# Kernel optimization log

Hardware: AMD Instinct MI355X
Metric: run time of the kernel (lower is better)

## Reference

```python
import jax, jax.numpy as jnp
import numpy as np

EPS = 1e-5
MODES = 64
KERNEL = 25
PRED = 336
N_ENC = 2

def rmsnorm(x, w):
    return x * jax.lax.rsqrt(jnp.mean(jnp.square(x), axis=-1, keepdims=True) + EPS) * w

def ffn(x, w1, b1, w2, b2):
    return jax.nn.gelu(x @ w1 + b1, approximate=False) @ w2 + b2

def series_decomp(x):
    # moving average with zero padding (Conv1d, kernel=KERNEL, weight=1/KERNEL)
    pad = (KERNEL - 1) // 2
    xp = jnp.pad(x, ((0, 0), (pad, pad), (0, 0)))
    cs = jnp.cumsum(xp, axis=1)
    cs = jnp.concatenate([jnp.zeros_like(cs[:, :1]), cs], axis=1)
    t = (cs[:, KERNEL:, :] - cs[:, :-KERNEL, :]) / KERNEL  # [B,T,C]
    return x - t, t

def fourier_block(x, w, nw):
    # x: [B,T,C]; w: [MODES,C,2] learned complex weights; nw: [C] rms scale
    B, T, C = x.shape
    Xf = jnp.fft.rfft(x, axis=1)                      # [B,F,C] complex64
    mag = jnp.sum(Xf[:, 1:].real**2 + Xf[:, 1:].imag**2, axis=-1)  # [B,F-1]
    K = min(MODES, Xf.shape[1] - 1)
    _, idx = jax.lax.top_k(mag, K)
    idx = idx + 1                                      # skip DC, [B,K]
    Xsel = jnp.take_along_axis(Xf, idx[:, :, None], axis=1)  # [B,K,C]
    Wc = w[:K, :, 0] + 1j * w[:K, :, 1]               # [K,C]
    Ysel = Xsel * Wc[None]                             # [B,K,C]
    Yf = jnp.zeros_like(Xf).at[jnp.arange(B)[:, None], idx].set(Ysel)
    y = jnp.fft.irfft(Yf, n=T, axis=1)                 # [B,T,C]
    return rmsnorm(y, nw)

def setup_inputs() -> dict:
    key = jax.random.key(0)
    ks = iter(jax.random.split(key, 64))
    B, L, Cin, Cout, D, FF = 32, 1024, 8, 8, 512, 2048
    r = lambda *s: jax.random.normal(next(ks), s, dtype=jnp.float32) * 0.02
    z = lambda *s: jnp.zeros(s, dtype=jnp.float32)
    o = lambda *s: jnp.ones(s, dtype=jnp.float32)
    return {
        'x': jax.random.normal(next(ks), (B, L, Cin), dtype=jnp.float32),
        'enc_in_w': r(Cin, D), 'enc_in_b': z(D),
        'dec_in_w': r(Cin, D), 'dec_in_b': z(D),
        'enc_freq_w': r(N_ENC, MODES, D, 2), 'enc_freq_nw': o(N_ENC, D),
        'enc_n1': o(N_ENC, D), 'enc_n2': o(N_ENC, D),
        'enc_w1': r(N_ENC, D, FF), 'enc_b1': z(N_ENC, FF),
        'enc_w2': r(N_ENC, FF, D), 'enc_b2': z(N_ENC, D),
        'dec_freq_w': r(MODES, D, 2), 'dec_freq_nw': o(D),
        'dec_n1': o(D), 'dec_n2': o(D), 'dec_nx': o(D),
        'dec_cross_w': r(D, D), 'dec_cross_b': z(D),
        'dec_w1': r(D, FF), 'dec_b1': z(FF),
        'dec_w2': r(FF, D), 'dec_b2': z(D),
        'seas_w': r(D, Cout), 'seas_b': z(Cout),
        'tr_w1': r(D, FF), 'tr_b1': z(FF),
        'tr_w2': r(FF, Cout), 'tr_b2': z(Cout),
        'mix_w': r(Cout, Cout), 'mix_b': z(Cout),
        'qpos': jax.random.normal(next(ks), (1, PRED, D), dtype=jnp.float32) * 0.02,
    }

def reference(x, enc_in_w, enc_in_b, dec_in_w, dec_in_b,
              enc_freq_w, enc_freq_nw, enc_n1, enc_n2, enc_w1, enc_b1, enc_w2, enc_b2,
              dec_freq_w, dec_freq_nw, dec_n1, dec_n2, dec_nx, dec_cross_w, dec_cross_b,
              dec_w1, dec_b1, dec_w2, dec_b2, seas_w, seas_b,
              tr_w1, tr_b1, tr_w2, tr_b2, mix_w, mix_b, qpos):
    s, t = series_decomp(x)
    sez = s @ enc_in_w + enc_in_b                      # [B,L,D]
    for i in range(N_ENC):
        sez = sez + fourier_block(rmsnorm(sez, enc_n1[i]), enc_freq_w[i], enc_freq_nw[i])
        sez = sez + ffn(rmsnorm(sez, enc_n2[i]), enc_w1[i], enc_b1[i], enc_w2[i], enc_b2[i])
    memory = sez
    tgt = qpos + sez[:, -1:, :]                        # [B,PRED,D]
    # decoder layer
    m = jnp.mean(memory, axis=1, keepdims=True)        # [B,1,D]
    m = rmsnorm(m, dec_nx) @ dec_cross_w + dec_cross_b
    y = fourier_block(rmsnorm(tgt, dec_n1), dec_freq_w, dec_freq_nw)
    xd = tgt + y * jax.nn.sigmoid(m)
    xd = xd + ffn(rmsnorm(xd, dec_n2), dec_w1, dec_b1, dec_w2, dec_b2)
    sez_out = xd @ seas_w + seas_b                     # [B,PRED,Cout]
    tr = t @ dec_in_w + dec_in_b
    tr_out = ffn(tr[:, -1:, :], tr_w1, tr_b1, tr_w2, tr_b2)  # [B,1,Cout], broadcasts
    out = sez_out + tr_out
    return out @ mix_w + mix_b
```

## Files before the change

### kernel.cpp

```cpp
#include <hip/hip_runtime.h>
#include <hip/hip_fp16.h>
#include <math.h>

#define B_    32
#define L_    1024
#define D_    512
#define FF_   2048
#define PRED_ 336
#define ME_   (B_*L_)
#define MD_   (B_*PRED_)
#define EPS_  1e-5f

typedef _Float16 f16;
typedef _Float16 f16x8 __attribute__((ext_vector_type(8)));
typedef float    f32x4 __attribute__((ext_vector_type(4)));

__device__ __forceinline__ float wred64(float v) {
#pragma unroll
  for (int o = 32; o > 0; o >>= 1) v += __shfl_xor(v, o, 64);
  return v;
}
__device__ __forceinline__ double dwred64(double v) {
#pragma unroll
  for (int o = 32; o > 0; o >>= 1) v += __shfl_xor(v, o, 64);
  return v;
}
__device__ __forceinline__ float gelu_f(float x) {
  return 0.5f * x * (1.0f + erff(x * 0.7071067811865476f));
}
__device__ __forceinline__ void gl2lds16(const void* g, void* l) {
  __builtin_amdgcn_global_load_lds((const __attribute__((address_space(1))) void*)g,
                                   (__attribute__((address_space(3))) void*)l, 16, 0, 0);
}

__global__ void k_transpose_cast(const float* __restrict__ in, f16* __restrict__ out, int R, int C) {
  __shared__ float t[32][33];
  int c0 = blockIdx.x * 32, r0 = blockIdx.y * 32;
  int tx = threadIdx.x, ty = threadIdx.y;
#pragma unroll
  for (int j = ty; j < 32; j += 8) t[j][tx] = in[(size_t)(r0 + j) * C + c0 + tx];
  __syncthreads();
#pragma unroll
  for (int j = ty; j < 32; j += 8) out[(size_t)(c0 + j) * R + r0 + tx] = (f16)t[tx][j];
}

__global__ __launch_bounds__(256) void k_decomp_proj(const float* __restrict__ x,
    const float* __restrict__ w, const float* __restrict__ bias, float* __restrict__ sez) {
  int b = blockIdx.x, t0 = blockIdx.y * 128, tid = threadIdx.x;
  __shared__ float xs[152][8];
  __shared__ float st[128][8];
  __shared__ float wsm[8 * 512];
  __shared__ float bs[512];
  for (int i = tid; i < 152 * 8; i += 256) {
    int tt = i >> 3, c = i & 7; int tg = t0 - 12 + tt;
    xs[tt][c] = (tg >= 0 && tg < 1024) ? x[((size_t)b * 1024 + tg) * 8 + c] : 0.0f;
  }
  for (int i = tid; i < 4096; i += 256) wsm[i] = w[i];
  for (int i = tid; i < 512; i += 256) bs[i] = bias[i];
  __syncthreads();
  for (int i = tid; i < 1024; i += 256) {
    int t = i >> 3, c = i & 7;
    float s = 0.f;
#pragma unroll
    for (int j = 0; j < 25; ++j) s += xs[t + j][c];
    st[t][c] = xs[t + 12][c] - s / 25.0f;
  }
  __syncthreads();
#pragma unroll
  for (int g = 0; g < 2; ++g) {
    int d = tid + g * 256;
    float wb[8];
#pragma unroll
    for (int c = 0; c < 8; ++c) wb[c] = wsm[c * 512 + d];
    float bb = bs[d];
    for (int t = 0; t < 128; ++t) {
      float o = bb;
#pragma unroll
      for (int c = 0; c < 8; ++c) o += st[t][c] * wb[c];
      sez[((size_t)b * 1024 + t0 + t) * 512 + d] = o;
    }
  }
}

__global__ __launch_bounds__(512) void k_trend_trin(const float* __restrict__ x, const float* __restrict__ w,
    const float* __restrict__ bias, float* __restrict__ trin) {
  int b = blockIdx.x, tid = threadIdx.x;
  __shared__ float tl[8];
  if (tid < 8) {
    float s = 0.f;
    for (int j = 1011; j <= 1023; ++j) s += x[((size_t)b * 1024 + j) * 8 + tid];
    tl[tid] = s / 25.0f;
  }
  __syncthreads();
  float acc = bias[tid];
#pragma unroll
  for (int c = 0; c < 8; ++c) acc += tl[c] * w[c * 512 + tid];
  trin[b * 512 + tid] = acc;
}

__global__ __launch_bounds__(256) void k_rinv(const float* __restrict__ xin, float* __restrict__ rinv) {
  int row = blockIdx.x * 4 + (threadIdx.x >> 6), lane = threadIdx.x & 63;
  const float4* p = (const float4*)(xin + (size_t)row * 512);
  float4 a = p[lane * 2], b = p[lane * 2 + 1];
  float ss = a.x*a.x + a.y*a.y + a.z*a.z + a.w*a.w + b.x*b.x + b.y*b.y + b.z*b.z + b.w*b.w;
  ss = wred64(ss);
  if (lane == 0) rinv[row] = rsqrtf(ss * (1.0f / 512.0f) + EPS_);
}

__global__ __launch_bounds__(256) void k_rms_f16(const float* __restrict__ xin, const float* __restrict__ w,
    f16* __restrict__ out) {
  int row = blockIdx.x * 4 + (threadIdx.x >> 6), lane = threadIdx.x & 63;
  const float4* p = (const float4*)(xin + (size_t)row * 512);
  float4 a = p[lane * 2], b = p[lane * 2 + 1];
  float ss = a.x*a.x + a.y*a.y + a.z*a.z + a.w*a.w + b.x*b.x + b.y*b.y + b.z*b.z + b.w*b.w;
  ss = wred64(ss);
  float ri = rsqrtf(ss * (1.0f / 512.0f) + EPS_);
  const float4* wp = (const float4*)w;
  float4 wa = wp[lane * 2], wb = wp[lane * 2 + 1];
  float va[8] = {a.x, a.y, a.z, a.w, b.x, b.y, b.z, b.w};
  float wv[8] = {wa.x, wa.y, wa.z, wa.w, wb.x, wb.y, wb.z, wb.w};
  f16x8 o;
#pragma unroll
  for (int j = 0; j < 8; ++j) o[j] = (f16)((va[j] * ri) * wv[j]);
  *(f16x8*)(out + (size_t)row * 512 + lane * 8) = o;
}

#define IDX_(i) ((i) + ((i) >> 4))
__global__ __launch_bounds__(256) void k_fft_enc(const float* __restrict__ sez, const float* __restrict__ rinv,
    const float* __restrict__ n1, float* __restrict__ Xf) {
  int b = blockIdx.x, c0 = blockIdx.y * 4, tid = threadIdx.x;
  __shared__ double Zr[2][1088], Zi[2][1088];
  __shared__ double TWr[256], TWi[256];
  if (tid < 256) {
    double a = -6.283185307179586232 * (double)tid / 1024.0;
    TWr[tid] = cos(a); TWi[tid] = sin(a);
  }
  for (int i = tid; i < 4096; i += 256) {
    int t = i >> 2, cl = i & 3;
    float xv = (sez[((size_t)b * 1024 + t) * 512 + c0 + cl] * rinv[b * 1024 + t]) * n1[c0 + cl];
    int u = t, rt = 0;
#pragma unroll
    for (int d = 0; d < 5; ++d) { rt = (rt << 2) | (u & 3); u >>= 2; }
    if (cl & 1) Zi[cl >> 1][IDX_(rt)] = (double)xv; else Zr[cl >> 1][IDX_(rt)] = (double)xv;
  }
  __syncthreads();
#pragma unroll
  for (int s = 0; s < 5; ++s) {
    const int lh = 2 * s, h = 1 << lh;
#pragma unroll
    for (int qi = 0; qi < 2; ++qi) {
      int q = tid + qi * 256;
      int p = q >> 8, qq = q & 255;
      int j = qq & (h - 1), g = qq >> lh;
      int p0 = (g << (lh + 2)) + j;
      int i0 = IDX_(p0), i1 = IDX_(p0 + h), i2 = IDX_(p0 + 2 * h), i3 = IDX_(p0 + 3 * h);
      int tw = j << (8 - lh);
      double w1r = TWr[tw], w1i = TWi[tw];
      double w2r = w1r * w1r - w1i * w1i, w2i = 2.0 * w1r * w1i;
      double w3r = w2r * w1r - w2i * w1i, w3i = w2r * w1i + w2i * w1r;
      double Ar = Zr[p][i0], Ai = Zi[p][i0];
      double br = Zr[p][i1], bi = Zi[p][i1];
      double cr = Zr[p][i2], ci = Zi[p][i2];
      double dr = Zr[p][i3], di = Zi[p][i3];
      double Br = br * w1r - bi * w1i, Bi = br * w1i + bi * w1r;
      double Cr = cr * w2r - ci * w2i, Ci = cr * w2i + ci * w2r;
      double Dr = dr * w3r - di * w3i, Di = dr * w3i + di * w3r;
      double T0r = Ar + Cr, T0i = Ai + Ci;
      double T1r = Ar - Cr, T1i = Ai - Ci;
      double T2r = Br + Dr, T2i = Bi + Di;
      double T3r = Bi - Di, T3i = Dr - Br;
      Zr[p][i0] = T0r + T2r; Zi[p][i0] = T0i + T2i;
      Zr[p][i1] = T1r + T3r; Zi[p][i1] = T1i + T3i;
      Zr[p][i2] = T0r - T2r; Zi[p][i2] = T0i - T2i;
      Zr[p][i3] = T1r - T3r; Zi[p][i3] = T1i - T3i;
    }
    __syncthreads();
  }
  for (int i = tid; i < 513 * 2; i += 256) {
    int f = i >> 1, p = i & 1;
    int mf = (1024 - f) & 1023;
    double Ar = Zr[p][IDX_(f)], Ai = Zi[p][IDX_(f)], Br = Zr[p][IDX_(mf)], Bi = Zi[p][IDX_(mf)];
    float4 o;
    o.x = (float)(0.5 * (Ar + Br)); o.y = (float)(0.5 * (Ai - Bi));
    o.z = (float)(0.5 * (Ai + Bi)); o.w = (float)(0.5 * (Br - Ar));
    *(float4*)&Xf[(((size_t)b * 513 + f) * 512 + c0 + 2 * p) * 2] = o;
  }
}

__global__ __launch_bounds__(256) void k_mag(const float* __restrict__ Xf, double* __restrict__ mag, int F) {
  int b = blockIdx.x, f = blockIdx.y + 1, tid = threadIdx.x;
  const float2* row = (const float2*)(Xf + ((size_t)b * F + f) * 512 * 2);
  double s = 0;
  for (int c = tid; c < 512; c += 256) { float2 v = row[c]; s += (double)v.x * v.x + (double)v.y * v.y; }
  s = dwred64(s);
  __shared__ double ps[4];
  if ((tid & 63) == 0) ps[tid >> 6] = s;
  __syncthreads();
  if (tid == 0) mag[b * 513 + f] = ps[0] + ps[1] + ps[2] + ps[3];
}

__global__ __launch_bounds__(256) void k_topk(const double* __restrict__ mag, int* __restrict__ idx, int F) {
  int b = blockIdx.x, tid = threadIdx.x;
  __shared__ double v[528];
  __shared__ double rv[256];
  __shared__ int ri[256];
  for (int s = tid; s < 528; s += 256) v[s] = (s >= 1 && s < F) ? mag[b * 513 + s] : -1e300;
  __syncthreads();
  for (int r = 0; r < 64; ++r) {
    double bv = -1e300; int bi = 0;
    for (int s = tid; s < 528; s += 256) { double xv = v[s]; if (xv > bv) { bv = xv; bi = s; } }
    rv[tid] = bv; ri[tid] = bi;
    __syncthreads();
    for (int st = 128; st > 0; st >>= 1) {
      if (tid < st) {
        double o = rv[tid + st]; int oi = ri[tid + st];
        if (o > rv[tid] || (o == rv[tid] && oi < ri[tid])) { rv[tid] = o; ri[tid] = oi; }
      }
      __syncthreads();
    }
    if (tid == 0) { idx[b * 64 + r] = ri[0]; v[ri[0]] = -1e300; }
    __syncthreads();
  }
}

__global__ __launch_bounds__(512) void k_gather(const float* __restrict__ Xf, const int* __restrict__ idx,
    const float* __restrict__ fw, float* __restrict__ Ysel, int F, int T) {
  int b = blockIdx.x, k = blockIdx.y, c = threadIdx.x;
  int f = idx[b * 64 + k];
  float sc = (2 * f == T) ? (1.0f / (float)T) : (2.0f / (float)T);
  float2 xv = *(const float2*)&Xf[(((size_t)b * F + f) * 512 + c) * 2];
  float wr = fw[(k * 512 + c) * 2], wi = fw[(k * 512 + c) * 2 + 1];
  float yr = (xv.x * wr - xv.y * wi) * sc;
  float yi = (xv.x * wi + xv.y * wr) * sc;
  *(float2*)&Ysel[((size_t)(b * 64 + k) * 512 + c) * 2] = make_float2(yr, yi);
}

template <int T>
__global__ __launch_bounds__(256) void k_irfft(const float* __restrict__ Ysel, const int* __restrict__ idx,
    const float* __restrict__ nw, const float* __restrict__ sig,
    float* __restrict__ dst, int mode) {
  int b = blockIdx.x, t0 = blockIdx.y * 16, tid = threadIdx.x;
  int cq = tid & 127;
  int tg = tid >> 7;
  __shared__ float tcT[16][68], tsT[16][68];
  __shared__ int sidx[64];
  __shared__ float red[4][8];
  __shared__ float rfac[16];
  if (tid < 64) sidx[tid] = idx[b * 64 + tid];
  __syncthreads();
  for (int i = tid; i < 1024; i += 256) {
    int k = i >> 4, tt = i & 15;
    int m = (sidx[k] * (t0 + tt)) % T;
    float ang = (float)m * (float)(6.283185307179586232 / (double)T);
    tcT[tt][k] = cosf(ang);
    tsT[tt][k] = sinf(ang);
  }
  __syncthreads();
  float acc[8][4];
#pragma unroll
  for (int q = 0; q < 8; ++q)
#pragma unroll
    for (int j = 0; j < 4; ++j) acc[q][j] = 0.f;
  const float4* ys = (const float4*)Ysel + (size_t)b * 64 * 256 + 2 * cq;
  for (int k4 = 0; k4 < 64; k4 += 4) {
    float4 ya[4], yb[4];
#pragma unroll
    for (int kk = 0; kk < 4; ++kk) {
      ya[kk] = ys[(size_t)(k4 + kk) * 256];
      yb[kk] = ys[(size_t)(k4 + kk) * 256 + 1];
    }
#pragma unroll
    for (int q = 0; q < 8; ++q) {
      int tt = tg * 8 + q;
      float4 c4 = *(const float4*)&tcT[tt][k4];
      float4 s4 = *(const float4*)&tsT[tt][k4];
      acc[q][0] += ya[0].x * c4.x - ya[0].y * s4.x;
      acc[q][1] += ya[0].z * c4.x - ya[0].w * s4.x;
      acc[q][2] += yb[0].x * c4.x - yb[0].y * s4.x;
      acc[q][3] += yb[0].z * c4.x - yb[0].w * s4.x;
      acc[q][0] += ya[1].x * c4.y - ya[1].y * s4.y;
      acc[q][1] += ya[1].z * c4.y - ya[1].w * s4.y;
      acc[q][2] += yb[1].x * c4.y - yb[1].y * s4.y;
      acc[q][3] += yb[1].z * c4.y - yb[1].w * s4.y;
      acc[q][0] += ya[2].x * c4.z - ya[2].y * s4.z;
      acc[q][1] += ya[2].z * c4.z - ya[2].w * s4.z;
      acc[q][2] += yb[2].x * c4.z - yb[2].y * s4.z;
      acc[q][3] += yb[2].z * c4.z - yb[2].w * s4.z;
      acc[q][0] += ya[3].x * c4.w - ya[3].y * s4.w;
      acc[q][1] += ya[3].z * c4.w - ya[3].w * s4.w;
      acc[q][2] += yb[3].x * c4.w - yb[3].y * s4.w;
      acc[q][3] += yb[3].z * c4.w - yb[3].w * s4.w;
    }
  }
  int lane = tid & 63, wv = tid >> 6;
#pragma unroll
  for (int q = 0; q < 8; ++q) {
    float v = wred64(acc[q][0] * acc[q][0] + acc[q][1] * acc[q][1]
                   + acc[q][2] * acc[q][2] + acc[q][3] * acc[q][3]);
    if (lane == 0) red[wv][q] = v;
  }
  __syncthreads();
  if (tid < 16) {
    int tg2 = tid >> 3, q = tid & 7;
    float s = red[tg2 * 2][q] + red[tg2 * 2 + 1][q];
    rfac[tid] = rsqrtf(s * (1.0f / 512.0f) + EPS_);
  }
  __syncthreads();
  int c = 4 * cq;
  float4 wc = *(const float4*)&nw[c];
  float4 sg = (mode == 1) ? *(const float4*)&sig[b * 512 + c] : make_float4(1.f, 1.f, 1.f, 1.f);
  float* drow = dst + ((size_t)b * T + t0) * 512 + c;
#pragma unroll
  for (int q = 0; q < 8; ++q) {
    int tt = tg * 8 + q;
    float rf = rfac[tt];
    float4 cur = *(float4*)&drow[(size_t)tt * 512];
    float y0 = (acc[q][0] * rf) * wc.x;
    float y1 = (acc[q][1] * rf) * wc.y;
    float y2 = (acc[q][2] * rf) * wc.z;
    float y3 = (acc[q][3] * rf) * wc.w;
    cur.x += (mode == 1) ? y0 * sg.x : y0;
    cur.y += (mode == 1) ? y1 * sg.y : y1;
    cur.z += (mode == 1) ? y2 * sg.z : y2;
    cur.w += (mode == 1) ? y3 * sg.w : y3;
    *(float4*)&drow[(size_t)tt * 512] = cur;
  }
}

template <int MODE>
__global__ __launch_bounds__(256) void k_gemm(const f16* __restrict__ A, const f16* __restrict__ Bt,
    const float* __restrict__ bias, float* __restrict__ Cf, f16* __restrict__ Ch, int M, int N, int K) {
  __shared__ f16 lA[128][64];
  __shared__ f16 lB[128][64];
  int bm = blockIdx.x, bn = blockIdx.y;
  int tid = threadIdx.x, lane = tid & 63, w = tid >> 6;
  int wr = w >> 1, wcq = w & 1;
  f32x4 acc[4][4];
#pragma unroll
  for (int i = 0; i < 4; ++i)
#pragma unroll
    for (int j = 0; j < 4; ++j) acc[i][j] = (f32x4){0.f, 0.f, 0.f, 0.f};
  int lr = lane >> 3;
  int kk = (lane & 7) * 8;
  int nk = K >> 6;
  for (int kt = 0; kt < nk; ++kt) {
    __syncthreads();
#pragma unroll
    for (int i = 0; i < 4; ++i) {
      int rt = (w * 4 + i) * 8;
      int rr = rt + lr;
      gl2lds16(A + (size_t)(bm * 128 + rr) * K + kt * 64 + kk, &lA[rt][0]);
      gl2lds16(Bt + (size_t)(bn * 128 + rr) * K + kt * 64 + kk, &lB[rt][0]);
    }
    __syncthreads();
#pragma unroll
    for (int ki = 0; ki < 2; ++ki) {
      f16x8 af[4], bf[4];
#pragma unroll
      for (int mi = 0; mi < 4; ++mi)
        af[mi] = *(const f16x8*)&lA[wr * 64 + mi * 16 + (lane & 15)][ki * 32 + (lane >> 4) * 8];
#pragma unroll
      for (int ni = 0; ni < 4; ++ni)
        bf[ni] = *(const f16x8*)&lB[wcq * 64 + ni * 16 + (lane & 15)][ki * 32 + (lane >> 4) * 8];
#pragma unroll
      for (int mi = 0; mi < 4; ++mi)
#pragma unroll
        for (int ni = 0; ni < 4; ++ni)
          acc[mi][ni] = __builtin_amdgcn_mfma_f32_16x16x32_f16(af[mi], bf[ni], acc[mi][ni], 0, 0, 0);
    }
  }
  int cbase = bn * 128 + wcq * 64;
  int rbase = bm * 128 + wr * 64;
#pragma unroll
  for (int mi = 0; mi < 4; ++mi)
#pragma unroll
    for (int ni = 0; ni < 4; ++ni) {
      int cg = cbase + ni * 16 + (lane & 15);
      float bv = bias[cg];
#pragma unroll
      for (int q = 0; q < 4; ++q) {
        int rg = rbase + mi * 16 + (lane >> 4) * 4 + q;
        float val = acc[mi][ni][q] + bv;
        if (MODE == 0) Ch[(size_t)rg * N + cg] = (f16)gelu_f(val);
        else           Cf[(size_t)rg * N + cg] += val;
      }
    }
}

__global__ __launch_bounds__(256) void k_mc_part(const float* __restrict__ sez, float* __restrict__ mcp) {
  int b = blockIdx.x, ch = blockIdx.y, tid = threadIdx.x;
  for (int d = tid; d < 512; d += 256) {
    float s = 0.f;
    for (int t = 0; t < 128; ++t) s += sez[((size_t)b * 1024 + ch * 128 + t) * 512 + d];
    mcp[((size_t)b * 8 + ch) * 512 + d] = s;
  }
}
__global__ __launch_bounds__(512) void k_mc_fin(const float* __restrict__ mcp, const float* __restrict__ nx,
    const float* __restrict__ Wc, const float* __restrict__ cb, float* __restrict__ sig) {
  int b = blockIdx.x, d = threadIdx.x;
  float m = 0.f;
#pragma unroll
  for (int ch = 0; ch < 8; ++ch) m += mcp[((size_t)b * 8 + ch) * 512 + d];
  m *= (1.0f / 1024.0f);
  float ss = wred64(m * m);
  __shared__ float ps[8];
  __shared__ float mn[512];
  int lane = d & 63, wv = d >> 6;
  if (lane == 0) ps[wv] = ss;
  __syncthreads();
  float tot = 0.f;
#pragma unroll
  for (int i = 0; i < 8; ++i) tot += ps[i];
  float ri = rsqrtf(tot * (1.0f / 512.0f) + EPS_);
  mn[d] = (m * ri) * nx[d];
  __syncthreads();
  float accv = cb[d];
  for (int e = 0; e < 512; ++e) accv += mn[e] * Wc[(size_t)e * 512 + d];
  sig[b * 512 + d] = 1.0f / (1.0f + expf(-accv));
}

__global__ __launch_bounds__(512) void k_make_tgt(const float* __restrict__ sez, const float* __restrict__ qpos,
    float* __restrict__ tgt, float* __restrict__ rinvd) {
  int row = blockIdx.x, d = threadIdx.x;
  int b = row / 336, p = row % 336;
  float v = qpos[(size_t)p * 512 + d] + sez[((size_t)b * 1024 + 1023) * 512 + d];
  tgt[(size_t)row * 512 + d] = v;
  float ss = wred64(v * v);
  __shared__ float ps[8];
  if ((d & 63) == 0) ps[d >> 6] = ss;
  __syncthreads();
  if (d == 0) {
    float t = 0.f;
#pragma unroll
    for (int i = 0; i < 8; ++i) t += ps[i];
    rinvd[row] = rsqrtf(t * (1.0f / 512.0f) + EPS_);
  }
}

__global__ void k_dtab(double* __restrict__ dtt) {
  int f = blockIdx.x;
  for (int t = threadIdx.x; t < 336; t += 256) {
    double cv = 0.0, sv = 0.0;
    if (f < 169) {
      int m = (f * t) % 336;
      double a = 6.283185307179586232 * (double)m / 336.0;
      cv = cos(a); sv = sin(a);
    }
    dtt[((size_t)t * 176 + f) * 2]     = cv;
    dtt[((size_t)t * 176 + f) * 2 + 1] = sv;
  }
}
__global__ __launch_bounds__(512) void k_dft_dec(const float* __restrict__ tgt, const float* __restrict__ rinvd,
    const float* __restrict__ n1, const double* __restrict__ dtt, float* __restrict__ Xf) {
  int b = blockIdx.x, f0 = blockIdx.y * 8, c = threadIdx.x;
  double ar[8], ai[8];
#pragma unroll
  for (int i = 0; i < 8; ++i) { ar[i] = 0.0; ai[i] = 0.0; }
  float nn = n1[c];
  const float* trow = tgt + (size_t)b * 336 * 512 + c;
  const float* rrow = rinvd + b * 336;
  for (int t = 0; t < 336; ++t) {
    float xv = (trow[(size_t)t * 512] * rrow[t]) * nn;
    double xd = (double)xv;
    const double* tab = dtt + ((size_t)t * 176 + f0) * 2;
#pragma unroll
    for (int ff = 0; ff < 8; ++ff) {
      ar[ff] += xd * tab[ff * 2];
      ai[ff] -= xd * tab[ff * 2 + 1];
    }
  }
#pragma unroll
  for (int ff = 0; ff < 8; ++ff) {
    int f = f0 + ff;
    if (f < 169)
      *(float2*)&Xf[(((size_t)b * 169 + f) * 512 + c) * 2] = make_float2((float)ar[ff], (float)ai[ff]);
  }
}

__global__ __launch_bounds__(256) void k_tr_h(const float* __restrict__ trin, const float* __restrict__ w1,
    const float* __restrict__ b1, float* __restrict__ H) {
  int b = blockIdx.x, j0 = blockIdx.y * 512, tid = threadIdx.x;
  __shared__ float xs[512];
  for (int i = tid; i < 512; i += 256) xs[i] = trin[b * 512 + i];
  __syncthreads();
  int j = j0 + tid;
  float h0 = b1[j], h1 = b1[j + 256];
  const float* wp = w1 + j;
#pragma unroll 4
  for (int e = 0; e < 512; ++e) {
    float xe = xs[e];
    h0 += xe * wp[(size_t)e * 2048];
    h1 += xe * wp[(size_t)e * 2048 + 256];
  }
  H[b * 2048 + j] = gelu_f(h0);
  H[b * 2048 + j + 256] = gelu_f(h1);
}

__global__ __launch_bounds__(256) void k_tr_red(const float* __restrict__ H, const float* __restrict__ w2,
    const float* __restrict__ b2, float* __restrict__ trout) {
  int b = blockIdx.x, tid = threadIdx.x;
  __shared__ float red[4][8];
  float part[8];
#pragma unroll
  for (int co = 0; co < 8; ++co) part[co] = 0.f;
#pragma unroll
  for (int jj = 0; jj < 8; ++jj) {
    int j = tid + jj * 256;
    float g = H[b * 2048 + j];
    float4 wa = *(const float4*)&w2[(size_t)j * 8];
    float4 wb = *(const float4*)&w2[(size_t)j * 8 + 4];
    part[0] += g * wa.x; part[1] += g * wa.y; part[2] += g * wa.z; part[3] += g * wa.w;
    part[4] += g * wb.x; part[5] += g * wb.y; part[6] += g * wb.z; part[7] += g * wb.w;
  }
  int lane = tid & 63, wv = tid >> 6;
#pragma unroll
  for (int co = 0; co < 8; ++co) {
    float v = wred64(part[co]);
    if (lane == 0) red[wv][co] = v;
  }
  __syncthreads();
  if (tid < 8) trout[b * 8 + tid] = red[0][tid] + red[1][tid] + red[2][tid] + red[3][tid] + b2[tid];
}

__global__ __launch_bounds__(256) void k_head(const float* __restrict__ xd, const float* __restrict__ sw,
    const float* __restrict__ sb, const float* __restrict__ trout, const float* __restrict__ mw,
    const float* __restrict__ mb, float* __restrict__ outp) {
  int row = blockIdx.x, tid = threadIdx.x;
  int b = row / 336;
  __shared__ float wsm[512 * 8];
  __shared__ float red[4][8];
  __shared__ float srow[8];
  for (int i = tid; i < 4096; i += 256) wsm[i] = sw[i];
  __syncthreads();
  float part[8];
#pragma unroll
  for (int co = 0; co < 8; ++co) part[co] = 0.f;
#pragma unroll
  for (int g = 0; g < 2; ++g) {
    int d = tid + g * 256;
    float xv = xd[(size_t)row * 512 + d];
#pragma unroll
    for (int co = 0; co < 8; ++co) part[co] += xv * wsm[d * 8 + co];
  }
  int lane = tid & 63, wv = tid >> 6;
#pragma unroll
  for (int co = 0; co < 8; ++co) {
    float v = wred64(part[co]);
    if (lane == 0) red[wv][co] = v;
  }
  __syncthreads();
  if (tid == 0) {
#pragma unroll
    for (int co = 0; co < 8; ++co)
      srow[co] = red[0][co] + red[1][co] + red[2][co] + red[3][co] + sb[co] + trout[b * 8 + co];
  }
  __syncthreads();
  if (tid < 8) {
    float o = mb[tid];
#pragma unroll
    for (int co = 0; co < 8; ++co) o += srow[co] * mw[co * 8 + tid];
    outp[(size_t)row * 8 + tid] = o;
  }
}

extern "C" void kernel_launch(void* const* d_in, const int* in_sizes, int n_in,
                              void* d_out, int out_size, void* d_ws, size_t ws_size,
                              hipStream_t stream) {
  const float* x        = (const float*)d_in[0];
  const float* enc_in_w = (const float*)d_in[1];
  const float* enc_in_b = (const float*)d_in[2];
  const float* dec_in_w = (const float*)d_in[3];
  const float* dec_in_b = (const float*)d_in[4];
  const float* enc_fw   = (const float*)d_in[5];
  const float* enc_fnw  = (const float*)d_in[6];
  const float* enc_n1   = (const float*)d_in[7];
  const float* enc_n2   = (const float*)d_in[8];
  const float* enc_w1   = (const float*)d_in[9];
  const float* enc_b1   = (const float*)d_in[10];
  const float* enc_w2   = (const float*)d_in[11];
  const float* enc_b2   = (const float*)d_in[12];
  const float* dec_fw   = (const float*)d_in[13];
  const float* dec_fnw  = (const float*)d_in[14];
  const float* dec_n1   = (const float*)d_in[15];
  const float* dec_n2   = (const float*)d_in[16];
  const float* dec_nx   = (const float*)d_in[17];
  const float* dec_cw   = (const float*)d_in[18];
  const float* dec_cb   = (const float*)d_in[19];
  const float* dec_w1   = (const float*)d_in[20];
  const float* dec_b1   = (const float*)d_in[21];
  const float* dec_w2   = (const float*)d_in[22];
  const float* dec_b2   = (const float*)d_in[23];
  const float* seas_w   = (const float*)d_in[24];
  const float* seas_b   = (const float*)d_in[25];
  const float* tr_w1    = (const float*)d_in[26];
  const float* tr_b1    = (const float*)d_in[27];
  const float* tr_w2    = (const float*)d_in[28];
  const float* tr_b2    = (const float*)d_in[29];
  const float* mix_w    = (const float*)d_in[30];
  const float* mix_b    = (const float*)d_in[31];
  const float* qpos     = (const float*)d_in[32];
  float* outp = (float*)d_out;
  (void)in_sizes; (void)n_in; (void)out_size; (void)ws_size;

  char* wsb = (char*)d_ws;
  size_t off = 0;
  auto take = [&](size_t n) -> char* {
    char* p = wsb + off;
    off = (off + n + 255) & ~(size_t)255;
    return p;
  };
  float*  sez   = (float*)take((size_t)ME_ * 512 * 4);
  f16*    xn    = (f16*)take((size_t)ME_ * 512 * 2);
  const size_t XF_BYTES = (size_t)32 * 513 * 512 * 2 * 4;
  char*   arena = take(XF_BYTES + (size_t)32 * 64 * 512 * 2 * 4);
  float*  Xf    = (float*)arena;
  f16*    hbuf  = (f16*)arena;
  float*  Ysel  = (float*)(arena + XF_BYTES);
  float*  tgt   = (float*)take((size_t)MD_ * 512 * 4);
  double* mag   = (double*)take((size_t)32 * 513 * 8);
  int*    idx   = (int*)take((size_t)32 * 64 * 4);
  float*  rinvp = (float*)take((size_t)ME_ * 4);
  float*  rinvd = (float*)take((size_t)MD_ * 4);
  float*  mcp   = (float*)take((size_t)32 * 8 * 512 * 4);
  float*  sig   = (float*)take((size_t)32 * 512 * 4);
  float*  trin  = (float*)take((size_t)32 * 512 * 4);
  float*  trout = (float*)take((size_t)32 * 8 * 4);
  float*  trH   = (float*)take((size_t)32 * 2048 * 4);
  double* dtt   = (double*)take((size_t)336 * 176 * 2 * 8);
  f16*    w1t   = (f16*)take((size_t)2 * 2048 * 512 * 2);
  f16*    w2t   = (f16*)take((size_t)2 * 512 * 2048 * 2);
  f16*    dw1t  = (f16*)take((size_t)2048 * 512 * 2);
  f16*    dw2t  = (f16*)take((size_t)512 * 2048 * 2);

  k_transpose_cast<<<dim3(64, 16), dim3(32, 8), 0, stream>>>(enc_w1, w1t, 512, 2048);
  k_transpose_cast<<<dim3(64, 16), dim3(32, 8), 0, stream>>>(enc_w1 + 512 * 2048, w1t + 2048 * 512, 512, 2048);
  k_transpose_cast<<<dim3(16, 64), dim3(32, 8), 0, stream>>>(enc_w2, w2t, 2048, 512);
  k_transpose_cast<<<dim3(16, 64), dim3(32, 8), 0, stream>>>(enc_w2 + 2048 * 512, w2t + 512 * 2048, 2048, 512);
  k_transpose_cast<<<dim3(64, 16), dim3(32, 8), 0, stream>>>(dec_w1, dw1t, 512, 2048);
  k_transpose_cast<<<dim3(16, 64), dim3(32, 8), 0, stream>>>(dec_w2, dw2t, 2048, 512);

  k_decomp_proj<<<dim3(32, 8), 256, 0, stream>>>(x, enc_in_w, enc_in_b, sez);
  k_trend_trin<<<32, 512, 0, stream>>>(x, dec_in_w, dec_in_b, trin);

  k_tr_h<<<dim3(32, 4), 256, 0, stream>>>(trin, tr_w1, tr_b1, trH);
  k_tr_red<<<32, 256, 0, stream>>>(trH, tr_w2, tr_b2, trout);

  for (int i = 0; i < 2; ++i) {
    k_rinv<<<ME_ / 4, 256, 0, stream>>>(sez, rinvp);
    k_fft_enc<<<dim3(32, 128), 256, 0, stream>>>(sez, rinvp, enc_n1 + i * 512, Xf);
    k_mag<<<dim3(32, 512), 256, 0, stream>>>(Xf, mag, 513);
    k_topk<<<32, 256, 0, stream>>>(mag, idx, 513);
    k_gather<<<dim3(32, 64), 512, 0, stream>>>(Xf, idx, enc_fw + (size_t)i * 64 * 512 * 2, Ysel, 513, 1024);
    k_irfft<1024><<<dim3(32, 64), 256, 0, stream>>>(Ysel, idx, enc_fnw + i * 512, nullptr, sez, 0);
    k_rms_f16<<<ME_ / 4, 256, 0, stream>>>(sez, enc_n2 + i * 512, xn);
    for (int ck = 0; ck < 2; ++ck) {
      const f16* Ax = xn + (size_t)ck * 16384 * 512;
      float* Cx = sez + (size_t)ck * 16384 * 512;
      k_gemm<0><<<dim3(128, 16), 256, 0, stream>>>(Ax, w1t + (size_t)i * 2048 * 512, enc_b1 + i * 2048,
                                                   nullptr, hbuf, 16384, 2048, 512);
      k_gemm<1><<<dim3(128, 4), 256, 0, stream>>>(hbuf, w2t + (size_t)i * 512 * 2048, enc_b2 + i * 512,
                                                  Cx, nullptr, 16384, 512, 2048);
    }
  }

  k_mc_part<<<dim3(32, 8), 256, 0, stream>>>(sez, mcp);
  k_mc_fin<<<32, 512, 0, stream>>>(mcp, dec_nx, dec_cw, dec_cb, sig);
  k_make_tgt<<<MD_, 512, 0, stream>>>(sez, qpos, tgt, rinvd);
  k_dtab<<<176, 256, 0, stream>>>(dtt);
  k_dft_dec<<<dim3(32, 22), 512, 0, stream>>>(tgt, rinvd, dec_n1, dtt, Xf);
  k_mag<<<dim3(32, 168), 256, 0, stream>>>(Xf, mag, 169);
  k_topk<<<32, 256, 0, stream>>>(mag, idx, 169);
  k_gather<<<dim3(32, 64), 512, 0, stream>>>(Xf, idx, dec_fw, Ysel, 169, 336);
  k_irfft<336><<<dim3(32, 21), 256, 0, stream>>>(Ysel, idx, dec_fnw, sig, tgt, 1);
  k_rms_f16<<<MD_ / 4, 256, 0, stream>>>(tgt, dec_n2, xn);
  k_gemm<0><<<dim3(84, 16), 256, 0, stream>>>(xn, dw1t, dec_b1, nullptr, hbuf, MD_, 2048, 512);
  k_gemm<1><<<dim3(84, 4), 256, 0, stream>>>(hbuf, dw2t, dec_b2, tgt, nullptr, MD_, 512, 2048);

  k_head<<<MD_, 256, 0, stream>>>(tgt, seas_w, seas_b, trout, mix_w, mix_b, outp);
}
```

Before: 1.613 ms.

## Remap GEMM workgroups XCD-aware and precompute normalized decoder input for DFT

The GEMM launch moves from a 2D grid to a 1D grid and remaps block IDs so that consecutive tiles (sharing A rows) land on the same XCD, which should improve L2 reuse across the eight chiplets. The decoder DFT now reads a pre-normalized tgt_n buffer written by k_make_tgt, dropping the per-element rinv and weight multiplies. It also computes 4 frequencies per block instead of 8, doubling the grid for more parallelism. This adds an extra MD×512 float buffer and write traffic. The remap assumes the grid size is divisible by 8.

```diff
diff --git a/kernel.cpp b/kernel.cpp
--- a/kernel.cpp
+++ b/kernel.cpp
@@ -329,10 +329,14 @@
 
 template <int MODE>
 __global__ __launch_bounds__(256) void k_gemm(const f16* __restrict__ A, const f16* __restrict__ Bt,
-    const float* __restrict__ bias, float* __restrict__ Cf, f16* __restrict__ Ch, int M, int N, int K) {
+    const float* __restrict__ bias, float* __restrict__ Cf, f16* __restrict__ Ch,
+    int M, int N, int K, int nbn) {
   __shared__ f16 lA[128][64];
   __shared__ f16 lB[128][64];
-  int bm = blockIdx.x, bn = blockIdx.y;
+  int nwg = gridDim.x;
+  int q8 = nwg >> 3;
+  int wgid = (blockIdx.x & 7) * q8 + (blockIdx.x >> 3);
+  int bm = wgid / nbn, bn = wgid - bm * nbn;
   int tid = threadIdx.x, lane = tid & 63, w = tid >> 6;
   int wr = w >> 1, wcq = w & 1;
   f32x4 acc[4][4];
@@ -420,7 +424,8 @@
 }
 
 __global__ __launch_bounds__(512) void k_make_tgt(const float* __restrict__ sez, const float* __restrict__ qpos,
-    float* __restrict__ tgt, float* __restrict__ rinvd) {
+    const float* __restrict__ n1, float* __restrict__ tgt, float* __restrict__ tgt_n,
+    float* __restrict__ rinvd) {
   int row = blockIdx.x, d = threadIdx.x;
   int b = row / 336, p = row % 336;
   float v = qpos[(size_t)p * 512 + d] + sez[((size_t)b * 1024 + 1023) * 512 + d];
@@ -429,12 +434,12 @@
   __shared__ float ps[8];
   if ((d & 63) == 0) ps[d >> 6] = ss;
   __syncthreads();
-  if (d == 0) {
-    float t = 0.f;
-#pragma unroll
-    for (int i = 0; i < 8; ++i) t += ps[i];
-    rinvd[row] = rsqrtf(t * (1.0f / 512.0f) + EPS_);
-  }
+  float t = 0.f;
+#pragma unroll
+  for (int i = 0; i < 8; ++i) t += ps[i];
+  float ri = rsqrtf(t * (1.0f / 512.0f) + EPS_);
+  tgt_n[(size_t)row * 512 + d] = (v * ri) * n1[d];
+  if (d == 0) rinvd[row] = ri;
 }
 
 __global__ void k_dtab(double* __restrict__ dtt) {
@@ -450,27 +455,24 @@
     dtt[((size_t)t * 176 + f) * 2 + 1] = sv;
   }
 }
-__global__ __launch_bounds__(512) void k_dft_dec(const float* __restrict__ tgt, const float* __restrict__ rinvd,
-    const float* __restrict__ n1, const double* __restrict__ dtt, float* __restrict__ Xf) {
-  int b = blockIdx.x, f0 = blockIdx.y * 8, c = threadIdx.x;
-  double ar[8], ai[8];
-#pragma unroll
-  for (int i = 0; i < 8; ++i) { ar[i] = 0.0; ai[i] = 0.0; }
-  float nn = n1[c];
-  const float* trow = tgt + (size_t)b * 336 * 512 + c;
-  const float* rrow = rinvd + b * 336;
+__global__ __launch_bounds__(512) void k_dft_dec(const float* __restrict__ tgt_n,
+    const double* __restrict__ dtt, float* __restrict__ Xf) {
+  int b = blockIdx.x, f0 = blockIdx.y * 4, c = threadIdx.x;
+  double ar[4], ai[4];
+#pragma unroll
+  for (int i = 0; i < 4; ++i) { ar[i] = 0.0; ai[i] = 0.0; }
+  const float* trow = tgt_n + (size_t)b * 336 * 512 + c;
   for (int t = 0; t < 336; ++t) {
-    float xv = (trow[(size_t)t * 512] * rrow[t]) * nn;
-    double xd = (double)xv;
+    double xd = (double)trow[(size_t)t * 512];
     const double* tab = dtt + ((size_t)t * 176 + f0) * 2;
 #pragma unroll
-    for (int ff = 0; ff < 8; ++ff) {
+    for (int ff = 0; ff < 4; ++ff) {
       ar[ff] += xd * tab[ff * 2];
       ai[ff] -= xd * tab[ff * 2 + 1];
     }
   }
 #pragma unroll
-  for (int ff = 0; ff < 8; ++ff) {
+  for (int ff = 0; ff < 4; ++ff) {
     int f = f0 + ff;
     if (f < 169)
       *(float2*)&Xf[(((size_t)b * 169 + f) * 512 + c) * 2] = make_float2((float)ar[ff], (float)ai[ff]);
@@ -617,6 +619,7 @@
   f16*    hbuf  = (f16*)arena;
   float*  Ysel  = (float*)(arena + XF_BYTES);
   float*  tgt   = (float*)take((size_t)MD_ * 512 * 4);
+  float*  tgt_n = (float*)take((size_t)MD_ * 512 * 4);
   double* mag   = (double*)take((size_t)32 * 513 * 8);
   int*    idx   = (int*)take((size_t)32 * 64 * 4);
   float*  rinvp = (float*)take((size_t)ME_ * 4);
@@ -656,25 +659,25 @@
     for (int ck = 0; ck < 2; ++ck) {
       const f16* Ax = xn + (size_t)ck * 16384 * 512;
       float* Cx = sez + (size_t)ck * 16384 * 512;
-      k_gemm<0><<<dim3(128, 16), 256, 0, stream>>>(Ax, w1t + (size_t)i * 2048 * 512, enc_b1 + i * 2048,
-                                                   nullptr, hbuf, 16384, 2048, 512);
-      k_gemm<1><<<dim3(128, 4), 256, 0, stream>>>(hbuf, w2t + (size_t)i * 512 * 2048, enc_b2 + i * 512,
-                                                  Cx, nullptr, 16384, 512, 2048);
+      k_gemm<0><<<128 * 16, 256, 0, stream>>>(Ax, w1t + (size_t)i * 2048 * 512, enc_b1 + i * 2048,
+                                              nullptr, hbuf, 16384, 2048, 512, 16);
+      k_gemm<1><<<128 * 4, 256, 0, stream>>>(hbuf, w2t + (size_t)i * 512 * 2048, enc_b2 + i * 512,
+                                             Cx, nullptr, 16384, 512, 2048, 4);
     }
   }
 
   k_mc_part<<<dim3(32, 8), 256, 0, stream>>>(sez, mcp);
   k_mc_fin<<<32, 512, 0, stream>>>(mcp, dec_nx, dec_cw, dec_cb, sig);
-  k_make_tgt<<<MD_, 512, 0, stream>>>(sez, qpos, tgt, rinvd);
+  k_make_tgt<<<MD_, 512, 0, stream>>>(sez, qpos, dec_n1, tgt, tgt_n, rinvd);
   k_dtab<<<176, 256, 0, stream>>>(dtt);
-  k_dft_dec<<<dim3(32, 22), 512, 0, stream>>>(tgt, rinvd, dec_n1, dtt, Xf);
+  k_dft_dec<<<dim3(32, 43), 512, 0, stream>>>(tgt_n, dtt, Xf);
   k_mag<<<dim3(32, 168), 256, 0, stream>>>(Xf, mag, 169);
   k_topk<<<32, 256, 0, stream>>>(mag, idx, 169);
   k_gather<<<dim3(32, 64), 512, 0, stream>>>(Xf, idx, dec_fw, Ysel, 169, 336);
   k_irfft<336><<<dim3(32, 21), 256, 0, stream>>>(Ysel, idx, dec_fnw, sig, tgt, 1);
   k_rms_f16<<<MD_ / 4, 256, 0, stream>>>(tgt, dec_n2, xn);
-  k_gemm<0><<<dim3(84, 16), 256, 0, stream>>>(xn, dw1t, dec_b1, nullptr, hbuf, MD_, 2048, 512);
-  k_gemm<1><<<dim3(84, 4), 256, 0, stream>>>(hbuf, dw2t, dec_b2, tgt, nullptr, MD_, 512, 2048);
+  k_gemm<0><<<84 * 16, 256, 0, stream>>>(xn, dw1t, dec_b1, nullptr, hbuf, MD_, 2048, 512, 16);
+  k_gemm<1><<<84 * 4, 256, 0, stream>>>(hbuf, dw2t, dec_b2, tgt, nullptr, MD_, 512, 2048, 4);
 
   k_head<<<MD_, 256, 0, stream>>>(tgt, seas_w, seas_b, trout, mix_w, mix_b, outp);
 }
```

Result: no change. 1.640 ms (+1.7%).
